# Performance work log

Hardware: AMD Instinct MI355X
Metric: run time of the kernel (lower is better)

The kernel has to match this reference:

```python
import jax, jax.numpy as jnp
import numpy as np

H = 1024      # hidden_dim == memory_dim (required by seq-axis concat)
M = 1024      # memory_dim
FF = 4096     # ff_dim
WIN = 16      # window_size
SLOTS = 10    # persistent memory slots
B, S = 2, 4096
EPS_LN = 1e-5
EPS_NORM = 1e-12


def _layernorm(x, g, b):
    m = jnp.mean(x, axis=-1, keepdims=True)
    v = jnp.var(x, axis=-1, keepdims=True)
    return (x - m) / jnp.sqrt(v + EPS_LN) * g + b


def setup_inputs() -> dict:
    key = jax.random.key(0)
    ks = jax.random.split(key, 12)

    def lin_w(k, out_d, in_d):
        return jax.random.normal(k, (out_d, in_d), jnp.float32) / np.sqrt(in_d)

    return {
        "x": jax.random.normal(ks[0], (B, S, H), jnp.float32),
        "mem_W": lin_w(ks[1], M, M), "mem_b": jnp.zeros((M,), jnp.float32),
        "P": jax.random.normal(ks[2], (SLOTS, M), jnp.float32),
        "Wi": lin_w(ks[3], M, H), "bi": jnp.zeros((M,), jnp.float32),
        "Wl1": lin_w(ks[4], M, M), "bl1": jnp.zeros((M,), jnp.float32),
        "Wl2": lin_w(ks[5], M, M), "bl2": jnp.zeros((M,), jnp.float32),
        "Wo": lin_w(ks[6], H, M), "bo": jnp.zeros((H,), jnp.float32),
        "fgate": jnp.ones((1,), jnp.float32),
        "lrate": jnp.ones((1,), jnp.float32),
        "Wg": lin_w(ks[7], H, 2 * H), "bg": jnp.zeros((H,), jnp.float32),
        "W1": lin_w(ks[8], FF, H), "b1": jnp.zeros((FF,), jnp.float32),
        "W2": lin_w(ks[9], H, FF), "b2": jnp.zeros((H,), jnp.float32),
        "g1": jnp.ones((H,), jnp.float32), "be1": jnp.zeros((H,), jnp.float32),
        "g2": jnp.ones((H,), jnp.float32), "be2": jnp.zeros((H,), jnp.float32),
        "g3": jnp.ones((H,), jnp.float32), "be3": jnp.zeros((H,), jnp.float32),
    }


def reference(x, mem_W, mem_b, P, Wi, bi, Wl1, bl1, Wl2, bl2, Wo, bo,
              fgate, lrate, Wg, bg, W1, b1, W2, b2,
              g1, be1, g2, be2, g3, be3):
    b, s, h = x.shape
    # k = concat(x, persistent) along seq; v = k.clone()
    k_full = jnp.concatenate([x, jnp.broadcast_to(P, (b,) + P.shape)], axis=1)  # [B, S+SLOTS, H]

    # sit at positions >= S and are never inside the window, so only x is attended.
    idx = jnp.arange(s)[:, None] + jnp.arange(-WIN, 1)[None, :]
    valid = idx >= 0
    k_win = k_full[:, jnp.maximum(idx, 0)]
    scores = jnp.einsum('bsh,bswh->bsw', x, k_win) * (h ** -0.5)
    scores = jnp.where(valid[None], scores, -jnp.inf)
    attn_out = jnp.einsum('bsw,bswh->bsh', jax.nn.softmax(scores, axis=-1), k_win)
    x1 = _layernorm(x + attn_out, g1, be1)

    # --- neural long-term memory (key == value since v = k.clone())
    kv = k_full.reshape(-1, h)
    kn = kv / jnp.maximum(jnp.linalg.norm(kv, axis=-1, keepdims=True), EPS_NORM)
    kp = kn @ Wi.T + bi          # projected key; value_proj is identical
    vp = kp
    hdd = jax.nn.silu(kp @ Wl1.T + bl1)
    hdd = jax.nn.silu(hdd @ Wl2.T + bl2)
    pred = hdd @ mem_W.T + mem_b
    diff = pred - vp
    n, m = diff.shape
    grad_W = (2.0 / (n * m)) * diff.T @ hdd          # d mse / d mem_W
    W_new = (1.0 - fgate) * mem_W + lrate * grad_W   # test-time memory update
    mem_out = hdd @ W_new.T + mem_b
    mo = (mem_out @ Wo.T + bo).reshape(b, -1, h)[:, :s]  # align with x seq length

    # --- gated fusion + FFN
    gate = jax.nn.sigmoid(jnp.concatenate([x1, mo], axis=-1) @ Wg.T + bg)
    combined = gate * x1 + (1.0 - gate) * mo
    x2 = _layernorm(x1 + combined, g2, be2)
    ff = jax.nn.silu(x2 @ W1.T + b1) @ W2.T + b2
    return _layernorm(x2 + ff, g3, be3)
```

## Files before the change

kernel.cpp:

```cpp
#include <hip/hip_runtime.h>
#include <hip/hip_bf16.h>

#define WIN 16
#define SLOTS 10
#define SS 4096
#define NTOK 8192
#define NKV 8212
#define NPOS 4106

typedef unsigned short u16;
typedef unsigned int u32;
typedef __attribute__((ext_vector_type(8))) short short8;
typedef __attribute__((ext_vector_type(4))) float f32x4;

__device__ __forceinline__ u16 f2bf(float f){
  union { float f; u32 u; } a; a.f = f;
  u32 r = (a.u + 0x7fff + ((a.u >> 16) & 1)) >> 16;
  return (u16)r;
}
__device__ __forceinline__ float bf2f(u16 v){
  union { u32 u; float f; } a; a.u = ((u32)v) << 16;
  return a.f;
}

#define GLOAD(gp, lp) __builtin_amdgcn_global_load_lds( \
    (const __attribute__((address_space(1))) void*)(gp), \
    (__attribute__((address_space(3))) void*)(lp), 16, 0, 0)

#define FENCE_BARRIER() do { \
    __builtin_amdgcn_sched_barrier(0); \
    __builtin_amdgcn_s_barrier(); \
    __builtin_amdgcn_sched_barrier(0); \
  } while(0)

__global__ __launch_bounds__(256) void cvt_all(
    const float4* __restrict__ s0, const float4* __restrict__ s1,
    const float4* __restrict__ s2, const float4* __restrict__ s3,
    const float4* __restrict__ s4, const float4* __restrict__ s5,
    const float4* __restrict__ s6, const float4* __restrict__ s7,
    ushort4* __restrict__ d0, ushort4* __restrict__ d1,
    ushort4* __restrict__ d2, ushort4* __restrict__ d3,
    ushort4* __restrict__ d4, ushort4* __restrict__ d5,
    ushort4* __restrict__ d6, ushort4* __restrict__ d7)
{
  int i = blockIdx.x * 256 + threadIdx.x;
  const float4* s; ushort4* d; int base;
  if      (i <  262144){ s=s0; d=d0; base=0; }
  else if (i <  524288){ s=s1; d=d1; base=262144; }
  else if (i <  786432){ s=s2; d=d2; base=524288; }
  else if (i < 1048576){ s=s3; d=d3; base=786432; }
  else if (i < 1310720){ s=s4; d=d4; base=1048576; }
  else if (i < 1835008){ s=s5; d=d5; base=1310720; }
  else if (i < 2883584){ s=s6; d=d6; base=1835008; }
  else                 { s=s7; d=d7; base=2883584; }
  float4 v = s[i - base];
  ushort4 o; o.x=f2bf(v.x); o.y=f2bf(v.y); o.z=f2bf(v.z); o.w=f2bf(v.w);
  d[i - base] = o;
}

__global__ __launch_bounds__(256) void attn_kv(
    const float* __restrict__ x, const float* __restrict__ P,
    const float* __restrict__ g1, const float* __restrict__ be1,
    u16* __restrict__ x1b, u16* __restrict__ kn)
{
  const int blk = blockIdx.x;
  const int t = threadIdx.x, lane = t & 63, w = t >> 6;
  if (blk >= NTOK){
    const int r = blk - NTOK;
    const int b = r / NPOS;
    const int pos = r - b*NPOS;
    const float* src = (pos < SS) ? (x + (((size_t)b*SS + pos) << 10))
                                  : (P + ((size_t)(pos - SS) << 10));
    float4 v = ((const float4*)src)[t];
    float s2 = v.x*v.x + v.y*v.y + v.z*v.z + v.w*v.w;
    #pragma unroll
    for (int off=32; off; off>>=1) s2 += __shfl_xor(s2, off, 64);
    __shared__ float sh[4];
    if (lane == 0) sh[w] = s2;
    __syncthreads();
    float S = sh[0]+sh[1]+sh[2]+sh[3];
    float inv = 1.f / fmaxf(sqrtf(S), 1e-12f);
    ushort4 o; o.x=f2bf(v.x*inv); o.y=f2bf(v.y*inv); o.z=f2bf(v.z*inv); o.w=f2bf(v.w*inv);
    ((ushort4*)kn)[((size_t)r << 8) + t] = o;
    return;
  }
  const int n = blk;
  const int b = n >> 12, s = n & 4095;
  const float* xb = x + ((size_t)b << 22);
  const float4 q = ((const float4*)(xb + ((size_t)s << 10)))[t];
  const int j0 = (s >= WIN) ? 0 : (WIN - s);
  float kvv[17][4];
  float part[17];
  #pragma unroll
  for (int j=0;j<17;j++){
    float4 kk = make_float4(0.f,0.f,0.f,0.f);
    if (j >= j0) kk = ((const float4*)(xb + ((size_t)(s - WIN + j) << 10)))[t];
    kvv[j][0]=kk.x; kvv[j][1]=kk.y; kvv[j][2]=kk.z; kvv[j][3]=kk.w;
    part[j] = q.x*kk.x + q.y*kk.y + q.z*kk.z + q.w*kk.w;
  }
  __shared__ float red[17][4];
  #pragma unroll
  for (int j=0;j<17;j++){
    float v = part[j];
    #pragma unroll
    for (int off=32; off; off>>=1) v += __shfl_xor(v, off, 64);
    if (lane == 0) red[j][w] = v;
  }
  __syncthreads();
  __shared__ float wsh[17];
  if (t == 0){
    float sc[17];
    float mx = -3.0e38f;
    #pragma unroll
    for (int j=0;j<17;j++){
      float v = (red[j][0]+red[j][1]+red[j][2]+red[j][3]) * 0.03125f;
      sc[j] = v;
      if (j >= j0) mx = fmaxf(mx, v);
    }
    float ssum = 0.f;
    #pragma unroll
    for (int j=0;j<17;j++){
      float e = (j >= j0) ? expf(sc[j]-mx) : 0.f;
      wsh[j] = e; ssum += e;
    }
    float inv = 1.f/ssum;
    #pragma unroll
    for (int j=0;j<17;j++) wsh[j] *= inv;
  }
  __syncthreads();
  float y0=q.x, y1=q.y, y2=q.z, y3=q.w;
  #pragma unroll
  for (int j=0;j<17;j++){
    float wj = wsh[j];
    y0 += wj*kvv[j][0]; y1 += wj*kvv[j][1]; y2 += wj*kvv[j][2]; y3 += wj*kvv[j][3];
  }
  float s1 = y0+y1+y2+y3;
  float s2 = y0*y0+y1*y1+y2*y2+y3*y3;
  #pragma unroll
  for (int off=32; off; off>>=1){ s1 += __shfl_xor(s1, off, 64); s2 += __shfl_xor(s2, off, 64); }
  __shared__ float rsh[8];
  if (lane == 0){ rsh[w] = s1; rsh[4+w] = s2; }
  __syncthreads();
  float S1 = rsh[0]+rsh[1]+rsh[2]+rsh[3];
  float S2 = rsh[4]+rsh[5]+rsh[6]+rsh[7];
  float mean = S1 * (1.f/1024.f);
  float var  = S2 * (1.f/1024.f) - mean*mean;
  float rstd = 1.f/sqrtf(var + 1e-5f);
  float4 gv = ((const float4*)g1)[t];
  float4 bv = ((const float4*)be1)[t];
  ushort4 ob;
  ob.x = f2bf((y0-mean)*rstd*gv.x + bv.x);
  ob.y = f2bf((y1-mean)*rstd*gv.y + bv.y);
  ob.z = f2bf((y2-mean)*rstd*gv.z + bv.z);
  ob.w = f2bf((y3-mean)*rstd*gv.w + bv.w);
  ((ushort4*)x1b)[((size_t)n << 8) + t] = ob;
}

template<int EPI, int SPLITA>
__global__ __launch_bounds__(256) void gemm_nt(
    const u16* __restrict__ A, const u16* __restrict__ A2,
    const u16* __restrict__ Bmat, const float* __restrict__ bias,
    const u16* __restrict__ auxb,
    float* __restrict__ Cf, u16* __restrict__ Cb,
    int N, int O, int ldA, int ldB, int klen)
{
  __shared__ __align__(16) u16 lA[4][128*32];
  __shared__ __align__(16) u16 lB[4][128*32];
  const int t = threadIdx.x;
  const int lane = t & 63;
  const int bm0 = blockIdx.x * 128;
  const int bn0 = blockIdx.y * 128;
  const int wid = t >> 6;
  const int wr = wid >> 1, wc = wid & 1;
  const int nkh = klen >> 5;

  f32x4 acc[4][4];
  #pragma unroll
  for (int i=0;i<4;i++)
    #pragma unroll
    for (int j=0;j<4;j++)
      acc[i][j] = (f32x4){0.f,0.f,0.f,0.f};

  const int srow = t >> 2;
  const int sch  = t & 3;
  const int csw  = ((sch ^ ((srow >> 1) & 3)) << 3);

  int gr0 = bm0 + srow;      gr0 = gr0 < N ? gr0 : N-1;
  int gr1 = bm0 + srow + 64; gr1 = gr1 < N ? gr1 : N-1;
  int gb0 = bn0 + srow;      gb0 = gb0 < O ? gb0 : O-1;
  int gb1 = bn0 + srow + 64; gb1 = gb1 < O ? gb1 : O-1;
  const u16* bA0 = A + (size_t)gr0*(size_t)ldA + csw;
  const u16* bA1 = A + (size_t)gr1*(size_t)ldA + csw;
  const u16* bA20 = SPLITA ? (A2 + ((size_t)gr0 << 10) + csw) : nullptr;
  const u16* bA21 = SPLITA ? (A2 + ((size_t)gr1 << 10) + csw) : nullptr;
  const u16* bB0 = Bmat + (size_t)gb0*(size_t)ldB + csw;
  const u16* bB1 = Bmat + (size_t)gb1*(size_t)ldB + csw;
  const int dLo = t << 3;
  const int dHi = (t << 3) + 2048;

  auto stage = [&](int j){
    const int kb = j << 5;
    const int s = j & 3;
    const u16* a0 = SPLITA ? ((kb < 1024) ? bA0 + kb : bA20 + (kb - 1024)) : bA0 + kb;
    const u16* a1 = SPLITA ? ((kb < 1024) ? bA1 + kb : bA21 + (kb - 1024)) : bA1 + kb;
    GLOAD(a0, &lA[s][dLo]);
    GLOAD(a1, &lA[s][dHi]);
    GLOAD(bB0 + kb, &lB[s][dLo]);
    GLOAD(bB1 + kb, &lB[s][dHi]);
  };

  stage(0);
  if (nkh > 1) stage(1);
  if (nkh > 2) stage(2);

  const int l15 = lane & 15;
  const int cq  = lane >> 4;
  const int soff = ((cq ^ ((l15 >> 1) & 3)) << 3);

  for (int j = 0; j < nkh; ++j){
    const int s = j & 3;
    const int cnt = 4*((j+1 < nkh) + (j+2 < nkh));
    if (cnt == 8)      { asm volatile("s_waitcnt vmcnt(8)" ::: "memory"); }
    else if (cnt == 4) { asm volatile("s_waitcnt vmcnt(4)" ::: "memory"); }
    else               { asm volatile("s_waitcnt vmcnt(0)" ::: "memory"); }
    FENCE_BARRIER();
    short8 af[4], bfv[4];
    #pragma unroll
    for (int mi=0;mi<4;mi++)
      af[mi] = *(const short8*)(&lA[s][((wr*64 + mi*16 + l15) * 32) + soff]);
    #pragma unroll
    for (int ni=0;ni<4;ni++)
      bfv[ni] = *(const short8*)(&lB[s][((wc*64 + ni*16 + l15) * 32) + soff]);
    if (j + 3 < nkh) stage(j + 3);
    __builtin_amdgcn_sched_barrier(0);
    __builtin_amdgcn_s_setprio(1);
    #pragma unroll
    for (int mi=0;mi<4;mi++)
      #pragma unroll
      for (int ni=0;ni<4;ni++)
        acc[mi][ni] = __builtin_amdgcn_mfma_f32_16x16x32_bf16(af[mi], bfv[ni], acc[mi][ni], 0, 0, 0);
    __builtin_amdgcn_s_setprio(0);
    __builtin_amdgcn_sched_barrier(0);
  }

  const int rbase = (lane >> 4) * 4;
  const int cidx = lane & 15;
  #pragma unroll
  for (int mi=0;mi<4;mi++){
    #pragma unroll
    for (int r=0;r<4;r++){
      const int n = bm0 + wr*64 + mi*16 + rbase + r;
      if (n >= N) continue;
      #pragma unroll
      for (int ni=0;ni<4;ni++){
        const int o = bn0 + wc*64 + ni*16 + cidx;
        float v = acc[mi][ni][r] + bias[o];
        if (EPI == 6){
          int b = n / NPOS;
          int pos = n - b*NPOS;
          if (pos < SS){
            Cb[(((size_t)(b*SS + pos)) << 10) + o] = f2bf(v);
          }
        } else {
          size_t idx = (size_t)n*(size_t)O + o;
          if (EPI == 0){ Cf[idx] = v; }
          else if (EPI == 1){ float sv = v/(1.f+__expf(-v)); Cb[idx] = f2bf(sv); }
          else if (EPI == 2){ Cb[idx] = f2bf(v); }
          else if (EPI == 4){ Cb[idx] = f2bf(v - bf2f(auxb[idx])); }
          else if (EPI == 5){ Cb[idx] = f2bf(1.f/(1.f+__expf(-v))); }
        }
      }
    }
  }
}

template<int EPI>
__global__ __launch_bounds__(512, 2) void gemm_256(
    const u16* __restrict__ A, const u16* __restrict__ Bmat,
    const float* __restrict__ bias,
    float* __restrict__ Cf, u16* __restrict__ Cb,
    int N, int O, int ldA, int ldB, int klen)
{
  __shared__ __align__(16) u16 lA[4][256*32];
  __shared__ __align__(16) u16 lB[4][256*32];
  const int t = threadIdx.x;
  const int lane = t & 63;
  const int wid = t >> 6;
  const int wr = wid >> 2, wc = wid & 3;
  const int bm0 = blockIdx.x * 256;
  const int bn0 = blockIdx.y * 256;
  const int nkh = (klen >> 6) * 2;

  f32x4 acc[8][4];
  #pragma unroll
  for (int i=0;i<8;i++)
    #pragma unroll
    for (int j=0;j<4;j++)
      acc[i][j] = (f32x4){0.f,0.f,0.f,0.f};

  const int srow = t >> 2;
  const int sch  = t & 3;
  const int csw  = ((sch ^ ((srow >> 1) & 3)) << 3);
  int gr0 = bm0 + srow;       gr0 = gr0 < N ? gr0 : N-1;
  int gr1 = bm0 + srow + 128; gr1 = gr1 < N ? gr1 : N-1;
  int gb0 = bn0 + srow;       gb0 = gb0 < O ? gb0 : O-1;
  int gb1 = bn0 + srow + 128; gb1 = gb1 < O ? gb1 : O-1;
  const u16* baseA0 = A    + (size_t)gr0*(size_t)ldA + csw;
  const u16* baseA1 = A    + (size_t)gr1*(size_t)ldA + csw;
  const u16* baseB0 = Bmat + (size_t)gb0*(size_t)ldB + csw;
  const u16* baseB1 = Bmat + (size_t)gb1*(size_t)ldB + csw;
  const int ldsLo = srow*32 + (sch << 3);
  const int ldsHi = (srow + 128)*32 + (sch << 3);

  auto stageA = [&](int j){
    const int kb = j << 5;
    const int s = j & 3;
    GLOAD(baseA0 + kb, &lA[s][ldsLo]);
    GLOAD(baseA1 + kb, &lA[s][ldsHi]);
  };
  auto stageB = [&](int j){
    const int kb = j << 5;
    const int s = j & 3;
    GLOAD(baseB0 + kb, &lB[s][ldsLo]);
    GLOAD(baseB1 + kb, &lB[s][ldsHi]);
  };

  stageA(0); stageB(0);
  if (nkh > 1){ stageA(1); stageB(1); }
  if (nkh > 2){ stageA(2); stageB(2); }

  const int l15 = lane & 15;
  const int cq  = lane >> 4;
  const int chS = ((cq ^ ((l15 >> 1) & 3)) << 3);

  for (int j = 0; j < nkh; ++j){
    const int s = j & 3;
    const int rem = nkh - 1 - j;
    if (rem >= 2)      { asm volatile("s_waitcnt vmcnt(8)" ::: "memory"); }
    else if (rem == 1) { asm volatile("s_waitcnt vmcnt(4)" ::: "memory"); }
    else               { asm volatile("s_waitcnt vmcnt(0)" ::: "memory"); }
    FENCE_BARRIER();
    short8 af[4], bfv[4];
    #pragma unroll
    for (int ni=0;ni<4;ni++)
      bfv[ni] = *(const short8*)(&lB[s][((wc*64 + ni*16 + l15) * 32) + chS]);
    #pragma unroll
    for (int mi=0;mi<4;mi++)
      af[mi] = *(const short8*)(&lA[s][((wr*128 + mi*16 + l15) * 32) + chS]);
    if (j + 3 < nkh) stageA(j + 3);
    __builtin_amdgcn_sched_barrier(0);
    __builtin_amdgcn_s_setprio(1);
    #pragma unroll
    for (int mi=0;mi<4;mi++)
      #pragma unroll
      for (int ni=0;ni<4;ni++)
        acc[mi][ni] = __builtin_amdgcn_mfma_f32_16x16x32_bf16(af[mi], bfv[ni], acc[mi][ni], 0, 0, 0);
    __builtin_amdgcn_s_setprio(0);
    __builtin_amdgcn_sched_barrier(0);
    FENCE_BARRIER();
    #pragma unroll
    for (int mi=0;mi<4;mi++)
      af[mi] = *(const short8*)(&lA[s][((wr*128 + (mi+4)*16 + l15) * 32) + chS]);
    if (j + 3 < nkh) stageB(j + 3);
    __builtin_amdgcn_sched_barrier(0);
    __builtin_amdgcn_s_setprio(1);
    #pragma unroll
    for (int mi=0;mi<4;mi++)
      #pragma unroll
      for (int ni=0;ni<4;ni++)
        acc[mi+4][ni] = __builtin_amdgcn_mfma_f32_16x16x32_bf16(af[mi], bfv[ni], acc[mi+4][ni], 0, 0, 0);
    __builtin_amdgcn_s_setprio(0);
    __builtin_amdgcn_sched_barrier(0);
  }

  const int rbase = (lane >> 4) * 4;
  const int cidx = lane & 15;
  #pragma unroll
  for (int mi=0;mi<8;mi++){
    #pragma unroll
    for (int r=0;r<4;r++){
      const int n = bm0 + wr*128 + mi*16 + rbase + r;
      if (n >= N) continue;
      #pragma unroll
      for (int ni=0;ni<4;ni++){
        const int o = bn0 + wc*64 + ni*16 + cidx;
        float v = acc[mi][ni][r] + bias[o];
        size_t idx = (size_t)n*(size_t)O + o;
        if (EPI == 0){ Cf[idx] = v; }
        else if (EPI == 1){ float sv = v/(1.f+__expf(-v)); Cb[idx] = f2bf(sv); }
        else if (EPI == 2){ Cb[idx] = f2bf(v); }
      }
    }
  }
}

#define NSPLIT 6
__global__ __launch_bounds__(256) void gemm_tn(
    const u16* __restrict__ A, const u16* __restrict__ B,
    float* __restrict__ part0, float* __restrict__ part1)
{
  __shared__ __align__(16) u16 lA[128*64];
  __shared__ __align__(16) u16 lB[128*64];
  const int t = threadIdx.x, lane = t & 63;
  const int i0 = blockIdx.x * 128, j0 = blockIdx.y * 128, z = blockIdx.z;
  const int wid = t >> 6, wr = wid >> 1, wc = wid & 1;
  const int TILES = (NKV + 63) >> 6;
  const int PER = (TILES + NSPLIT - 1) / NSPLIT;
  const int kt0 = z * PER;
  const int ktend = (kt0 + PER < TILES) ? (kt0 + PER) : TILES;

  f32x4 acc[4][4];
  #pragma unroll
  for (int i=0;i<4;i++)
    #pragma unroll
    for (int j=0;j<4;j++)
      acc[i][j] = (f32x4){0.f,0.f,0.f,0.f};

  const int p = t & 31;
  const int g = t >> 5;

  auto loadr = [&](int kt, short8 R[8]){
    const int n0 = kt << 6;
    const int na = n0 + 2*p, nb = na + 1;
    short8 z8 = (short8){0,0,0,0,0,0,0,0};
    R[0]=z8;R[1]=z8;R[2]=z8;R[3]=z8;R[4]=z8;R[5]=z8;R[6]=z8;R[7]=z8;
    if (na < NKV){
      const u16* ra = A + (size_t)na*1024 + i0 + g*16;
      R[0] = *(const short8*)ra; R[1] = *(const short8*)(ra+8);
      const u16* rb = B + (size_t)na*1024 + j0 + g*16;
      R[4] = *(const short8*)rb; R[5] = *(const short8*)(rb+8);
    }
    if (nb < NKV){
      const u16* ra = A + (size_t)nb*1024 + i0 + g*16;
      R[2] = *(const short8*)ra; R[3] = *(const short8*)(ra+8);
      const u16* rb = B + (size_t)nb*1024 + j0 + g*16;
      R[6] = *(const short8*)rb; R[7] = *(const short8*)(rb+8);
    }
  };

  short8 cr[8], nr[8];
  loadr(kt0, cr);

  const int pc = p >> 2, pl = p & 3;

  for (int kt = kt0; kt < ktend; ++kt){
    if (kt + 1 < ktend) loadr(kt + 1, nr);
    asm volatile("" ::: "memory");
    FENCE_BARRIER();
    u32* wA = (u32*)lA; u32* wB = (u32*)lB;
    #pragma unroll
    for (int e=0;e<8;e++){
      const int s = (pc ^ e) * 4 + pl;
      wA[(g*16 + e)*32 + s]     = ((u32)(u16)cr[0][e]) | (((u32)(u16)cr[2][e]) << 16);
      wB[(g*16 + e)*32 + s]     = ((u32)(u16)cr[4][e]) | (((u32)(u16)cr[6][e]) << 16);
    }
    #pragma unroll
    for (int e=0;e<8;e++){
      const int s = (pc ^ e) * 4 + pl;
      wA[(g*16 + 8 + e)*32 + s] = ((u32)(u16)cr[1][e]) | (((u32)(u16)cr[3][e]) << 16);
      wB[(g*16 + 8 + e)*32 + s] = ((u32)(u16)cr[5][e]) | (((u32)(u16)cr[7][e]) << 16);
    }
    asm volatile("s_waitcnt lgkmcnt(0)" ::: "memory");
    FENCE_BARRIER();
    const int l15 = lane & 15;
    const int rx = l15 & 7;
    const int cq = lane >> 4;
    #pragma unroll
    for (int kk=0;kk<2;kk++){
      const int soff = (((kk*4 + cq) ^ rx) << 3);
      short8 af[4], bfv[4];
      #pragma unroll
      for (int mi=0;mi<4;mi++)
        af[mi] = *(const short8*)(lA + ((wr*64 + mi*16 + l15) << 6) + soff);
      #pragma unroll
      for (int ni=0;ni<4;ni++)
        bfv[ni] = *(const short8*)(lB + ((wc*64 + ni*16 + l15) << 6) + soff);
      #pragma unroll
      for (int mi=0;mi<4;mi++)
        #pragma unroll
        for (int ni=0;ni<4;ni++)
          acc[mi][ni] = __builtin_amdgcn_mfma_f32_16x16x32_bf16(af[mi], bfv[ni], acc[mi][ni], 0, 0, 0);
    }
    #pragma unroll
    for (int e=0;e<8;e++) cr[e] = nr[e];
  }

  float* dst = (z < 4) ? (part0 + ((size_t)z << 20)) : (part1 + ((size_t)(z-4) << 20));
  const int rbase = (lane >> 4) * 4;
  const int cidx = lane & 15;
  #pragma unroll
  for (int mi=0;mi<4;mi++)
    #pragma unroll
    for (int r=0;r<4;r++){
      const int i = i0 + wr*64 + mi*16 + rbase + r;
      #pragma unroll
      for (int ni=0;ni<4;ni++){
        const int j = j0 + wc*64 + ni*16 + cidx;
        dst[((size_t)i << 10) + j] = acc[mi][ni][r];
      }
    }
}

__global__ __launch_bounds__(256) void wnew_k(const float* __restrict__ part0,
                                              const float* __restrict__ part1,
                                              const float* __restrict__ memW,
                                              const float* __restrict__ fg,
                                              const float* __restrict__ lr,
                                              u16* __restrict__ out)
{
  int i = blockIdx.x*256 + threadIdx.x;
  float s = part0[i] + part0[i + (1<<20)] + part0[i + (2<<20)] + part0[i + (3<<20)]
          + part1[i] + part1[i + (1<<20)];
  const float scale = 2.f / ((float)NKV * 1024.f);
  float v = (1.f - fg[0])*memW[i] + lr[0]*scale*s;
  out[i] = f2bf(v);
}

__global__ __launch_bounds__(256) void ln_gate(
    const u16* __restrict__ x1b, const u16* __restrict__ gateb,
    const u16* __restrict__ mob, const float* __restrict__ g2,
    const float* __restrict__ be2, u16* __restrict__ x2b)
{
  const int n = blockIdx.x;
  const int t = threadIdx.x, lane = t & 63, w = t >> 6;
  const size_t rb = (size_t)n << 8;
  ushort4 xa = ((const ushort4*)x1b)[rb+t];
  ushort4 ga = ((const ushort4*)gateb)[rb+t];
  ushort4 ma = ((const ushort4*)mob)[rb+t];
  float a0=bf2f(xa.x),a1=bf2f(xa.y),a2=bf2f(xa.z),a3=bf2f(xa.w);
  float g0=bf2f(ga.x),g1v=bf2f(ga.y),g2v=bf2f(ga.z),g3v=bf2f(ga.w);
  float m0=bf2f(ma.x),m1=bf2f(ma.y),m2=bf2f(ma.z),m3=bf2f(ma.w);
  float y0 = a0 + g0*a0 + (1.f-g0)*m0;
  float y1 = a1 + g1v*a1 + (1.f-g1v)*m1;
  float y2 = a2 + g2v*a2 + (1.f-g2v)*m2;
  float y3 = a3 + g3v*a3 + (1.f-g3v)*m3;
  float s1 = y0+y1+y2+y3;
  float s2 = y0*y0+y1*y1+y2*y2+y3*y3;
  #pragma unroll
  for (int off=32; off; off>>=1){ s1 += __shfl_xor(s1, off, 64); s2 += __shfl_xor(s2, off, 64); }
  __shared__ float rsh[8];
  if (lane == 0){ rsh[w] = s1; rsh[4+w] = s2; }
  __syncthreads();
  float S1 = rsh[0]+rsh[1]+rsh[2]+rsh[3];
  float S2 = rsh[4]+rsh[5]+rsh[6]+rsh[7];
  float mean = S1 * (1.f/1024.f);
  float var  = S2 * (1.f/1024.f) - mean*mean;
  float rstd = 1.f/sqrtf(var + 1e-5f);
  float4 gv = ((const float4*)g2)[t];
  float4 bv = ((const float4*)be2)[t];
  ushort4 ob;
  ob.x = f2bf((y0-mean)*rstd*gv.x + bv.x);
  ob.y = f2bf((y1-mean)*rstd*gv.y + bv.y);
  ob.z = f2bf((y2-mean)*rstd*gv.z + bv.z);
  ob.w = f2bf((y3-mean)*rstd*gv.w + bv.w);
  ((ushort4*)x2b)[rb + t] = ob;
}

__global__ __launch_bounds__(256) void ln_final(
    const u16* __restrict__ x2b, const float* __restrict__ g3,
    const float* __restrict__ be3, float* __restrict__ out)
{
  const int n = blockIdx.x;
  const int t = threadIdx.x, lane = t & 63, w = t >> 6;
  const size_t rb = (size_t)n << 8;
  ushort4 xa = ((const ushort4*)x2b)[rb+t];
  float4 f = ((const float4*)out)[rb+t];
  float y0 = bf2f(xa.x)+f.x, y1 = bf2f(xa.y)+f.y, y2 = bf2f(xa.z)+f.z, y3 = bf2f(xa.w)+f.w;
  float s1 = y0+y1+y2+y3;
  float s2 = y0*y0+y1*y1+y2*y2+y3*y3;
  #pragma unroll
  for (int off=32; off; off>>=1){ s1 += __shfl_xor(s1, off, 64); s2 += __shfl_xor(s2, off, 64); }
  __shared__ float rsh[8];
  if (lane == 0){ rsh[w] = s1; rsh[4+w] = s2; }
  __syncthreads();
  float S1 = rsh[0]+rsh[1]+rsh[2]+rsh[3];
  float S2 = rsh[4]+rsh[5]+rsh[6]+rsh[7];
  float mean = S1 * (1.f/1024.f);
  float var  = S2 * (1.f/1024.f) - mean*mean;
  float rstd = 1.f/sqrtf(var + 1e-5f);
  float4 gv = ((const float4*)g3)[t];
  float4 bv = ((const float4*)be3)[t];
  float4 o;
  o.x = (y0-mean)*rstd*gv.x + bv.x;
  o.y = (y1-mean)*rstd*gv.y + bv.y;
  o.z = (y2-mean)*rstd*gv.z + bv.z;
  o.w = (y3-mean)*rstd*gv.w + bv.w;
  ((float4*)out)[rb + t] = o;
}

extern "C" void kernel_launch(void* const* d_in, const int* in_sizes, int n_in,
                              void* d_out, int out_size, void* d_ws, size_t ws_size,
                              hipStream_t stream)
{
  const float* x    = (const float*)d_in[0];
  const float* memW = (const float*)d_in[1];
  const float* memb = (const float*)d_in[2];
  const float* P    = (const float*)d_in[3];
  const float* Wi   = (const float*)d_in[4];
  const float* bi   = (const float*)d_in[5];
  const float* Wl1  = (const float*)d_in[6];
  const float* bl1  = (const float*)d_in[7];
  const float* Wl2  = (const float*)d_in[8];
  const float* bl2  = (const float*)d_in[9];
  const float* Wo   = (const float*)d_in[10];
  const float* bo   = (const float*)d_in[11];
  const float* fg   = (const float*)d_in[12];
  const float* lr   = (const float*)d_in[13];
  const float* Wg   = (const float*)d_in[14];
  const float* bg   = (const float*)d_in[15];
  const float* W1   = (const float*)d_in[16];
  const float* b1   = (const float*)d_in[17];
  const float* W2   = (const float*)d_in[18];
  const float* b2   = (const float*)d_in[19];
  const float* g1   = (const float*)d_in[20];
  const float* be1  = (const float*)d_in[21];
  const float* g2   = (const float*)d_in[22];
  const float* be2  = (const float*)d_in[23];
  const float* g3   = (const float*)d_in[24];
  const float* be3  = (const float*)d_in[25];
  float* out = (float*)d_out;

  const size_t SZ_TOK = (size_t)NTOK*1024*2;
  const size_t SZ_KV  = (size_t)NKV*1024*2;
  char* base = (char*)d_ws;
  size_t off = 0;
  auto alloc = [&](size_t bytes) -> char* {
    char* p = base + off;
    off += (bytes + 255) & ~(size_t)255;
    return p;
  };
  u16* x1b   = (u16*)alloc(SZ_TOK);
  u16* knb   = (u16*)alloc(SZ_KV);
  u16* h1b   = (u16*)alloc(SZ_KV);
  u16* hddb  = (u16*)alloc(SZ_KV);
  u16* kpb   = (u16*)alloc(SZ_KV);
  u16* wnewb = (u16*)alloc((size_t)1024*1024*2);
  u16* WiB   = (u16*)alloc((size_t)1024*1024*2);
  u16* Wl1B  = (u16*)alloc((size_t)1024*1024*2);
  u16* Wl2B  = (u16*)alloc((size_t)1024*1024*2);
  u16* memWB = (u16*)alloc((size_t)1024*1024*2);
  u16* WoB   = (u16*)alloc((size_t)1024*1024*2);
  u16* WgB   = (u16*)alloc((size_t)1024*2048*2);
  u16* W1B   = (u16*)alloc((size_t)4096*1024*2);
  u16* W2B   = (u16*)alloc((size_t)1024*4096*2);
  if (ws_size < off) return;

  u16*   diffb   = knb;
  float* part0   = (float*)kpb;
  float* part1   = (float*)WiB;
  u16*   memoutb = knb;
  u16*   mob     = h1b;
  u16*   gateb   = hddb;
  u16*   x2b     = kpb;
  u16*   ff1b    = x1b;

  cvt_all<<<15360, 256, 0, stream>>>(
      (const float4*)Wi, (const float4*)Wl1, (const float4*)Wl2, (const float4*)memW,
      (const float4*)Wo, (const float4*)Wg, (const float4*)W1, (const float4*)W2,
      (ushort4*)WiB, (ushort4*)Wl1B, (ushort4*)Wl2B, (ushort4*)memWB,
      (ushort4*)WoB, (ushort4*)WgB, (ushort4*)W1B, (ushort4*)W2B);

  attn_kv<<<NTOK + NKV, 256, 0, stream>>>(x, P, g1, be1, x1b, knb);

  dim3 gkv(65, 8, 1);
  gemm_nt<2,0><<<gkv, 256, 0, stream>>>(knb, nullptr, WiB, bi, nullptr, nullptr, kpb, NKV, 1024, 1024, 1024, 1024);
  gemm_nt<1,0><<<gkv, 256, 0, stream>>>(kpb, nullptr, Wl1B, bl1, nullptr, nullptr, h1b, NKV, 1024, 1024, 1024, 1024);
  gemm_nt<1,0><<<gkv, 256, 0, stream>>>(h1b, nullptr, Wl2B, bl2, nullptr, nullptr, hddb, NKV, 1024, 1024, 1024, 1024);
  gemm_nt<4,0><<<gkv, 256, 0, stream>>>(hddb, nullptr, memWB, memb, kpb, nullptr, diffb, NKV, 1024, 1024, 1024, 1024);
  gemm_tn<<<dim3(8, 8, NSPLIT), 256, 0, stream>>>(diffb, hddb, part0, part1);
  wnew_k<<<4096, 256, 0, stream>>>(part0, part1, memW, fg, lr, wnewb);
  gemm_nt<2,0><<<gkv, 256, 0, stream>>>(hddb, nullptr, wnewb, memb, nullptr, nullptr, memoutb, NKV, 1024, 1024, 1024, 1024);
  gemm_nt<6,0><<<gkv, 256, 0, stream>>>(memoutb, nullptr, WoB, bo, nullptr, nullptr, mob, NKV, 1024, 1024, 1024, 1024);
  gemm_nt<5,1><<<dim3(64, 8, 1), 256, 0, stream>>>(x1b, mob, WgB, bg, nullptr, nullptr, gateb, NTOK, 1024, 1024, 2048, 2048);
  ln_gate<<<NTOK, 256, 0, stream>>>(x1b, gateb, mob, g2, be2, x2b);
  gemm_256<1><<<dim3(32, 16, 1), 512, 0, stream>>>(x2b, W1B, b1, nullptr, ff1b, NTOK, 4096, 1024, 1024, 1024);
  gemm_nt<0,0><<<dim3(64, 8, 1), 256, 0, stream>>>(ff1b, nullptr, W2B, b2, nullptr, out, nullptr, NTOK, 1024, 4096, 4096, 4096);
  ln_final<<<NTOK, 256, 0, stream>>>(x2b, g3, be3, out);
}
```

Baseline: 630.3 us.

## Split-K FF2 GEMM on 256-tile kernel and merge weight conversion into prep kernel

Merges the weight-conversion kernel and the attention/key-normalisation kernel into a single launch. It also replaces the FF2 GEMM (K=4096) with the 256x256-tile kernel run as a 2-way split-K, writing two fp32 partials. A new final layernorm kernel sums the partials with the bias and residual. This trades two extra fp32 partial buffers (more memory traffic) for better occupancy and larger tiles on the FF2 GEMM, and falls back to the old path if workspace is too small.

```diff
diff --git a/kernel.cpp b/kernel.cpp
--- a/kernel.cpp
+++ b/kernel.cpp
@@ -7,6 +7,7 @@
 #define NTOK 8192
 #define NKV 8212
 #define NPOS 4106
+#define CVTBLKS 15360
 
 typedef unsigned short u16;
 typedef unsigned int u32;
@@ -33,40 +34,39 @@
     __builtin_amdgcn_sched_barrier(0); \
   } while(0)
 
-__global__ __launch_bounds__(256) void cvt_all(
-    const float4* __restrict__ s0, const float4* __restrict__ s1,
-    const float4* __restrict__ s2, const float4* __restrict__ s3,
-    const float4* __restrict__ s4, const float4* __restrict__ s5,
-    const float4* __restrict__ s6, const float4* __restrict__ s7,
-    ushort4* __restrict__ d0, ushort4* __restrict__ d1,
-    ushort4* __restrict__ d2, ushort4* __restrict__ d3,
-    ushort4* __restrict__ d4, ushort4* __restrict__ d5,
-    ushort4* __restrict__ d6, ushort4* __restrict__ d7)
-{
-  int i = blockIdx.x * 256 + threadIdx.x;
-  const float4* s; ushort4* d; int base;
-  if      (i <  262144){ s=s0; d=d0; base=0; }
-  else if (i <  524288){ s=s1; d=d1; base=262144; }
-  else if (i <  786432){ s=s2; d=d2; base=524288; }
-  else if (i < 1048576){ s=s3; d=d3; base=786432; }
-  else if (i < 1310720){ s=s4; d=d4; base=1048576; }
-  else if (i < 1835008){ s=s5; d=d5; base=1310720; }
-  else if (i < 2883584){ s=s6; d=d6; base=1835008; }
-  else                 { s=s7; d=d7; base=2883584; }
-  float4 v = s[i - base];
-  ushort4 o; o.x=f2bf(v.x); o.y=f2bf(v.y); o.z=f2bf(v.z); o.w=f2bf(v.w);
-  d[i - base] = o;
-}
-
-__global__ __launch_bounds__(256) void attn_kv(
+__global__ __launch_bounds__(256) void prep(
+    const float4* __restrict__ cs0, const float4* __restrict__ cs1,
+    const float4* __restrict__ cs2, const float4* __restrict__ cs3,
+    const float4* __restrict__ cs4, const float4* __restrict__ cs5,
+    const float4* __restrict__ cs6, const float4* __restrict__ cs7,
+    ushort4* __restrict__ cd0, ushort4* __restrict__ cd1,
+    ushort4* __restrict__ cd2, ushort4* __restrict__ cd3,
+    ushort4* __restrict__ cd4, ushort4* __restrict__ cd5,
+    ushort4* __restrict__ cd6, ushort4* __restrict__ cd7,
     const float* __restrict__ x, const float* __restrict__ P,
     const float* __restrict__ g1, const float* __restrict__ be1,
     u16* __restrict__ x1b, u16* __restrict__ kn)
 {
   const int blk = blockIdx.x;
   const int t = threadIdx.x, lane = t & 63, w = t >> 6;
-  if (blk >= NTOK){
-    const int r = blk - NTOK;
+  if (blk < CVTBLKS){
+    int i = blk * 256 + t;
+    const float4* s; ushort4* d; int base;
+    if      (i <  262144){ s=cs0; d=cd0; base=0; }
+    else if (i <  524288){ s=cs1; d=cd1; base=262144; }
+    else if (i <  786432){ s=cs2; d=cd2; base=524288; }
+    else if (i < 1048576){ s=cs3; d=cd3; base=786432; }
+    else if (i < 1310720){ s=cs4; d=cd4; base=1048576; }
+    else if (i < 1835008){ s=cs5; d=cd5; base=1310720; }
+    else if (i < 2883584){ s=cs6; d=cd6; base=1835008; }
+    else                 { s=cs7; d=cd7; base=2883584; }
+    float4 v = s[i - base];
+    ushort4 o; o.x=f2bf(v.x); o.y=f2bf(v.y); o.z=f2bf(v.z); o.w=f2bf(v.w);
+    d[i - base] = o;
+    return;
+  }
+  if (blk >= CVTBLKS + NTOK){
+    const int r = blk - CVTBLKS - NTOK;
     const int b = r / NPOS;
     const int pos = r - b*NPOS;
     const float* src = (pos < SS) ? (x + (((size_t)b*SS + pos) << 10))
@@ -84,7 +84,7 @@
     ((ushort4*)kn)[((size_t)r << 8) + t] = o;
     return;
   }
-  const int n = blk;
+  const int n = blk - CVTBLKS;
   const int b = n >> 12, s = n & 4095;
   const float* xb = x + ((size_t)b << 22);
   const float4 q = ((const float4*)(xb + ((size_t)s << 10)))[t];
@@ -278,7 +278,7 @@
 __global__ __launch_bounds__(512, 2) void gemm_256(
     const u16* __restrict__ A, const u16* __restrict__ Bmat,
     const float* __restrict__ bias,
-    float* __restrict__ Cf, u16* __restrict__ Cb,
+    float* __restrict__ Cf, float* __restrict__ Cf2, u16* __restrict__ Cb,
     int N, int O, int ldA, int ldB, int klen)
 {
   __shared__ __align__(16) u16 lA[4][256*32];
@@ -289,7 +289,8 @@
   const int wr = wid >> 2, wc = wid & 3;
   const int bm0 = blockIdx.x * 256;
   const int bn0 = blockIdx.y * 256;
-  const int nkh = (klen >> 6) * 2;
+  const size_t koff = (size_t)blockIdx.z * (size_t)klen;
+  const int nkh = klen >> 5;
 
   f32x4 acc[8][4];
   #pragma unroll
@@ -305,10 +306,10 @@
   int gr1 = bm0 + srow + 128; gr1 = gr1 < N ? gr1 : N-1;
   int gb0 = bn0 + srow;       gb0 = gb0 < O ? gb0 : O-1;
   int gb1 = bn0 + srow + 128; gb1 = gb1 < O ? gb1 : O-1;
-  const u16* baseA0 = A    + (size_t)gr0*(size_t)ldA + csw;
-  const u16* baseA1 = A    + (size_t)gr1*(size_t)ldA + csw;
-  const u16* baseB0 = Bmat + (size_t)gb0*(size_t)ldB + csw;
-  const u16* baseB1 = Bmat + (size_t)gb1*(size_t)ldB + csw;
+  const u16* baseA0 = A    + (size_t)gr0*(size_t)ldA + koff + csw;
+  const u16* baseA1 = A    + (size_t)gr1*(size_t)ldA + koff + csw;
+  const u16* baseB0 = Bmat + (size_t)gb0*(size_t)ldB + koff + csw;
+  const u16* baseB1 = Bmat + (size_t)gb1*(size_t)ldB + koff + csw;
   const int ldsLo = srow*32 + (sch << 3);
   const int ldsHi = (srow + 128)*32 + (sch << 3);
 
@@ -373,6 +374,7 @@
     __builtin_amdgcn_sched_barrier(0);
   }
 
+  float* dstf = (EPI == 7) ? (blockIdx.z ? Cf2 : Cf) : Cf;
   const int rbase = (lane >> 4) * 4;
   const int cidx = lane & 15;
   #pragma unroll
@@ -384,11 +386,14 @@
       #pragma unroll
       for (int ni=0;ni<4;ni++){
         const int o = bn0 + wc*64 + ni*16 + cidx;
-        float v = acc[mi][ni][r] + bias[o];
         size_t idx = (size_t)n*(size_t)O + o;
-        if (EPI == 0){ Cf[idx] = v; }
-        else if (EPI == 1){ float sv = v/(1.f+__expf(-v)); Cb[idx] = f2bf(sv); }
-        else if (EPI == 2){ Cb[idx] = f2bf(v); }
+        if (EPI == 7){ dstf[idx] = acc[mi][ni][r]; }
+        else {
+          float v = acc[mi][ni][r] + bias[o];
+          if (EPI == 0){ Cf[idx] = v; }
+          else if (EPI == 1){ float sv = v/(1.f+__expf(-v)); Cb[idx] = f2bf(sv); }
+          else if (EPI == 2){ Cb[idx] = f2bf(v); }
+        }
       }
     }
   }
@@ -566,6 +571,43 @@
   ushort4 xa = ((const ushort4*)x2b)[rb+t];
   float4 f = ((const float4*)out)[rb+t];
   float y0 = bf2f(xa.x)+f.x, y1 = bf2f(xa.y)+f.y, y2 = bf2f(xa.z)+f.z, y3 = bf2f(xa.w)+f.w;
+  float s1 = y0+y1+y2+y3;
+  float s2 = y0*y0+y1*y1+y2*y2+y3*y3;
+  #pragma unroll
+  for (int off=32; off; off>>=1){ s1 += __shfl_xor(s1, off, 64); s2 += __shfl_xor(s2, off, 64); }
+  __shared__ float rsh[8];
+  if (lane == 0){ rsh[w] = s1; rsh[4+w] = s2; }
+  __syncthreads();
+  float S1 = rsh[0]+rsh[1]+rsh[2]+rsh[3];
+  float S2 = rsh[4]+rsh[5]+rsh[6]+rsh[7];
+  float mean = S1 * (1.f/1024.f);
+  float var  = S2 * (1.f/1024.f) - mean*mean;
+  float rstd = 1.f/sqrtf(var + 1e-5f);
+  float4 gv = ((const float4*)g3)[t];
+  float4 bv = ((const float4*)be3)[t];
+  float4 o;
+  o.x = (y0-mean)*rstd*gv.x + bv.x;
+  o.y = (y1-mean)*rstd*gv.y + bv.y;
+  o.z = (y2-mean)*rstd*gv.z + bv.z;
+  o.w = (y3-mean)*rstd*gv.w + bv.w;
+  ((float4*)out)[rb + t] = o;
+}
+
+__global__ __launch_bounds__(256) void ln_final2(
+    const u16* __restrict__ x2b, const float* __restrict__ p0,
+    const float* __restrict__ p1, const float* __restrict__ b2,
+    const float* __restrict__ g3, const float* __restrict__ be3,
+    float* __restrict__ out)
+{
+  const int n = blockIdx.x;
+  const int t = threadIdx.x, lane = t & 63, w = t >> 6;
+  const size_t rb = (size_t)n << 8;
+  ushort4 xa = ((const ushort4*)x2b)[rb+t];
+  float4 f0 = ((const float4*)p0)[rb+t];
+  float4 f1 = ((const float4*)p1)[rb+t];
+  float4 bb = ((const float4*)b2)[t];
+  float y0 = bf2f(xa.x)+f0.x+f1.x+bb.x, y1 = bf2f(xa.y)+f0.y+f1.y+bb.y;
+  float y2 = bf2f(xa.z)+f0.z+f1.z+bb.z, y3 = bf2f(xa.w)+f0.w+f1.w+bb.w;
   float s1 = y0+y1+y2+y3;
   float s2 = y0*y0+y1*y1+y2*y2+y3*y3;
   #pragma unroll
@@ -643,7 +685,12 @@
   u16* WgB   = (u16*)alloc((size_t)1024*2048*2);
   u16* W1B   = (u16*)alloc((size_t)4096*1024*2);
   u16* W2B   = (u16*)alloc((size_t)1024*4096*2);
-  if (ws_size < off) return;
+  const size_t off_base = off;
+  if (ws_size < off_base) return;
+
+  float* ffp0 = (float*)alloc((size_t)NTOK*1024*4);
+  float* ffp1 = (float*)alloc((size_t)NTOK*1024*4);
+  const bool use_split_ff2 = (ws_size >= off);
 
   u16*   diffb   = knb;
   float* part0   = (float*)kpb;
@@ -654,13 +701,12 @@
   u16*   x2b     = kpb;
   u16*   ff1b    = x1b;
 
-  cvt_all<<<15360, 256, 0, stream>>>(
+  prep<<<CVTBLKS + NTOK + NKV, 256, 0, stream>>>(
       (const float4*)Wi, (const float4*)Wl1, (const float4*)Wl2, (const float4*)memW,
       (const float4*)Wo, (const float4*)Wg, (const float4*)W1, (const float4*)W2,
       (ushort4*)WiB, (ushort4*)Wl1B, (ushort4*)Wl2B, (ushort4*)memWB,
-      (ushort4*)WoB, (ushort4*)WgB, (ushort4*)W1B, (ushort4*)W2B);
-
-  attn_kv<<<NTOK + NKV, 256, 0, stream>>>(x, P, g1, be1, x1b, knb);
+      (ushort4*)WoB, (ushort4*)WgB, (ushort4*)W1B, (ushort4*)W2B,
+      x, P, g1, be1, x1b, knb);
 
   dim3 gkv(65, 8, 1);
   gemm_nt<2,0><<<gkv, 256, 0, stream>>>(knb, nullptr, WiB, bi, nullptr, nullptr, kpb, NKV, 1024, 1024, 1024, 1024);
@@ -673,7 +719,12 @@
   gemm_nt<6,0><<<gkv, 256, 0, stream>>>(memoutb, nullptr, WoB, bo, nullptr, nullptr, mob, NKV, 1024, 1024, 1024, 1024);
   gemm_nt<5,1><<<dim3(64, 8, 1), 256, 0, stream>>>(x1b, mob, WgB, bg, nullptr, nullptr, gateb, NTOK, 1024, 1024, 2048, 2048);
   ln_gate<<<NTOK, 256, 0, stream>>>(x1b, gateb, mob, g2, be2, x2b);
-  gemm_256<1><<<dim3(32, 16, 1), 512, 0, stream>>>(x2b, W1B, b1, nullptr, ff1b, NTOK, 4096, 1024, 1024, 1024);
-  gemm_nt<0,0><<<dim3(64, 8, 1), 256, 0, stream>>>(ff1b, nullptr, W2B, b2, nullptr, out, nullptr, NTOK, 1024, 4096, 4096, 4096);
-  ln_final<<<NTOK, 256, 0, stream>>>(x2b, g3, be3, out);
-}
+  gemm_256<1><<<dim3(32, 16, 1), 512, 0, stream>>>(x2b, W1B, b1, nullptr, nullptr, ff1b, NTOK, 4096, 1024, 1024, 1024);
+  if (use_split_ff2){
+    gemm_256<7><<<dim3(32, 4, 2), 512, 0, stream>>>(ff1b, W2B, nullptr, ffp0, ffp1, nullptr, NTOK, 1024, 4096, 4096, 2048);
+    ln_final2<<<NTOK, 256, 0, stream>>>(x2b, ffp0, ffp1, b2, g3, be3, out);
+  } else {
+    gemm_nt<0,0><<<dim3(64, 8, 1), 256, 0, stream>>>(ff1b, nullptr, W2B, b2, nullptr, out, nullptr, NTOK, 1024, 4096, 4096, 4096);
+    ln_final<<<NTOK, 256, 0, stream>>>(x2b, g3, be3, out);
+  }
+}
```

Result: slower. 665.7 us (+5.6%).
